# Optimization experiments

Hardware: AMD Instinct MI355X
Metric: run time of the kernel (lower is better)

Reference implementation:

```python
import jax, jax.numpy as jnp
import numpy as np

N_ATOMS = 100_000   # atom_node.size(0)
N_EDGES = 3_200_000  # avg degree 32


def setup_inputs() -> dict:
    key = jax.random.key(0)
    k1, k2, k3, k4, k5 = jax.random.split(key, 5)
    disp = jax.random.normal(k1, (N_EDGES, 3), dtype=jnp.float32)
    a = jax.random.normal(k2, (N_EDGES,), dtype=jnp.float32)
    b = jax.random.normal(k3, (N_EDGES,), dtype=jnp.float32)
    edge_index = jax.random.randint(k4, (2, N_EDGES), 0, N_ATOMS, dtype=jnp.int64)
    atom_node = jax.random.randint(k5, (N_ATOMS,), 0, 100, dtype=jnp.int64)
    return {"disp": disp, "a": a, "b": b, "edge_index": edge_index, "atom_node": atom_node}


def _energy(disp, a, b):
    # surrogate differentiable per-edge energy: E = sum_e a_e*r2_e + b_e*exp(-r2_e)
    r2 = jnp.sum(disp * disp, axis=-1)  # [E]
    return jnp.sum(a * r2 + b * jnp.exp(-r2))


def reference(disp, a, b, edge_index, atom_node):
    n = atom_node.shape[0]
    # force = -dE/d(disp), create_graph analog: jax grads are differentiable
    force_edge = -jax.grad(_energy, argnums=0)(disp, a, b)  # [E,3]
    # dual scatter-add over the two endpoint index rows, then subtract
    f_src = jax.ops.segment_sum(force_edge, edge_index[0], num_segments=n)  # [N,3]
    f_dst = jax.ops.segment_sum(force_edge, edge_index[1], num_segments=n)  # [N,3]
    return f_src - f_dst
```

## Files before the change

kernel.cpp:

```cpp
#include <hip/hip_runtime.h>
#include <hip/hip_bf16.h>
#include <hip/hip_fp16.h>
#include <math.h>
#include <stdint.h>

constexpr int TPB         = 256;
constexpr int U           = 8;
constexpr int EPB         = TPB * U;
constexpr int RECS        = EPB * 2;
constexpr int NPB_SHIFT   = 10;
constexpr int NODES_PER_B = 1 << NPB_SHIFT;
constexpr int NB_MAX      = 128;
constexpr int CAP         = 56;
constexpr int SPLIT       = 8;
constexpr int OCAP        = 262144;

__device__ __forceinline__ uint64_t pack_rec(int local, float fx, float fy, float fz) {
    uint64_t hx = __half_as_ushort(__float2half(fx));
    uint64_t hy = __half_as_ushort(__float2half(fy));
    uint64_t hz = __half_as_ushort(__float2half(fz));
    return (uint64_t)(unsigned)local | (hx << 16) | (hy << 32) | (hz << 48);
}

__global__ void __launch_bounds__(TPB)
p1_partition(const float* __restrict__ disp,
             const float* __restrict__ a,
             const float* __restrict__ b,
             const int* __restrict__ src,
             const int* __restrict__ dst,
             uint64_t* __restrict__ grecords,
             uint4* __restrict__ ovf,
             int* __restrict__ ovf_cnt,
             int E, int NB, int NBLK) {
    __shared__ int      s_cnt[NB_MAX];
    __shared__ int      s_off[NB_MAX];
    __shared__ int      s_gd[NB_MAX];
    __shared__ uint64_t s_rec[RECS];
    __shared__ uint8_t  s_bin[RECS];

    const int t = threadIdx.x;
    const int blk = blockIdx.x;
    const int base = blk * EPB;
    const int bend = min(base + EPB, E);

    if (t < NB_MAX) s_cnt[t] = 0;
    __syncthreads();

    const int e0 = base + t * U;
    float dxv[U], dyv[U], dzv[U], av[U], bv[U];
    int sv[U], dv[U];
    bool valid[U];
    if (e0 + U <= bend) {
        const float4* p = (const float4*)(disp + (size_t)3 * e0);
        float4 q0 = p[0], q1 = p[1], q2 = p[2];
        float4 q3 = p[3], q4 = p[4], q5 = p[5];
        dxv[0] = q0.x; dyv[0] = q0.y; dzv[0] = q0.z;
        dxv[1] = q0.w; dyv[1] = q1.x; dzv[1] = q1.y;
        dxv[2] = q1.z; dyv[2] = q1.w; dzv[2] = q2.x;
        dxv[3] = q2.y; dyv[3] = q2.z; dzv[3] = q2.w;
        dxv[4] = q3.x; dyv[4] = q3.y; dzv[4] = q3.z;
        dxv[5] = q3.w; dyv[5] = q4.x; dzv[5] = q4.y;
        dxv[6] = q4.z; dyv[6] = q4.w; dzv[6] = q5.x;
        dxv[7] = q5.y; dyv[7] = q5.z; dzv[7] = q5.w;
        float4 qa0 = *(const float4*)(a + e0);
        float4 qa1 = *(const float4*)(a + e0 + 4);
        av[0] = qa0.x; av[1] = qa0.y; av[2] = qa0.z; av[3] = qa0.w;
        av[4] = qa1.x; av[5] = qa1.y; av[6] = qa1.z; av[7] = qa1.w;
        float4 qb0 = *(const float4*)(b + e0);
        float4 qb1 = *(const float4*)(b + e0 + 4);
        bv[0] = qb0.x; bv[1] = qb0.y; bv[2] = qb0.z; bv[3] = qb0.w;
        bv[4] = qb1.x; bv[5] = qb1.y; bv[6] = qb1.z; bv[7] = qb1.w;
        int4 qs0 = *(const int4*)(src + e0);
        int4 qs1 = *(const int4*)(src + e0 + 4);
        sv[0] = qs0.x; sv[1] = qs0.y; sv[2] = qs0.z; sv[3] = qs0.w;
        sv[4] = qs1.x; sv[5] = qs1.y; sv[6] = qs1.z; sv[7] = qs1.w;
        int4 qd0 = *(const int4*)(dst + e0);
        int4 qd1 = *(const int4*)(dst + e0 + 4);
        dv[0] = qd0.x; dv[1] = qd0.y; dv[2] = qd0.z; dv[3] = qd0.w;
        dv[4] = qd1.x; dv[5] = qd1.y; dv[6] = qd1.z; dv[7] = qd1.w;
#pragma unroll
        for (int u = 0; u < U; ++u) valid[u] = true;
    } else {
#pragma unroll
        for (int u = 0; u < U; ++u) {
            int e = e0 + u;
            valid[u] = (e < bend);
            if (valid[u]) {
                dxv[u] = disp[3 * e + 0];
                dyv[u] = disp[3 * e + 1];
                dzv[u] = disp[3 * e + 2];
                av[u] = a[e]; bv[u] = b[e];
                sv[u] = src[e]; dv[u] = dst[e];
            }
        }
    }

    uint64_t rec[2 * U];
    int meta[2 * U];
#pragma unroll
    for (int u = 0; u < U; ++u) {
        if (valid[u]) {
            float dx = dxv[u], dy = dyv[u], dz = dzv[u];
            float r2 = dx * dx + dy * dy + dz * dz;
            float coef = -2.0f * (av[u] - bv[u] * __expf(-r2));
            float fx = coef * dx, fy = coef * dy, fz = coef * dz;
            int nds[2] = { sv[u], dv[u] };
#pragma unroll
            for (int j = 0; j < 2; ++j) {
                int k = 2 * u + j;
                float s = j ? -1.0f : 1.0f;
                int node = nds[j];
                rec[k] = pack_rec(node & (NODES_PER_B - 1), s * fx, s * fy, s * fz);
                int bin = node >> NPB_SHIFT;
                int rank = atomicAdd(&s_cnt[bin], 1);
                meta[k] = (bin << 16) | rank;
            }
        } else {
            meta[2 * u] = -1; meta[2 * u + 1] = -1;
        }
    }
    __syncthreads();

    if (t < 64) {
        int v0 = s_cnt[t];
        int v1 = s_cnt[64 + t];
#pragma unroll
        for (int d = 1; d < 64; d <<= 1) {
            int u0 = __shfl_up(v0, d, 64);
            int u1 = __shfl_up(v1, d, 64);
            if (t >= d) { v0 += u0; v1 += u1; }
        }
        int total0 = __shfl(v0, 63, 64);
        s_off[t] = v0;
        s_off[64 + t] = v1 + total0;
    }
    __syncthreads();

    if (t < NB) {
        s_gd[t] = s_cnt[t] - s_off[t];
    }
#pragma unroll
    for (int k = 0; k < 2 * U; ++k) {
        if (meta[k] >= 0) {
            int bin = meta[k] >> 16;
            int rank = meta[k] & 0xFFFF;
            int pos = s_off[bin] - s_cnt[bin] + rank;
            s_rec[pos] = rec[k];
            s_bin[pos] = (uint8_t)bin;
        }
    }
    __syncthreads();

    if (t < NB) {
        uint64_t* seg = grecords + ((size_t)t * NBLK + blk) * CAP;
        for (int p = s_cnt[t]; p < CAP; ++p) seg[p] = 0ull;
    }

    const int total = s_off[NB_MAX - 1];
    for (int i = t; i < total; i += TPB) {
        uint64_t q = s_rec[i];
        int bin = (int)s_bin[i];
        int pos = s_gd[bin] + i;
        if ((unsigned)pos < (unsigned)CAP) {
            grecords[((size_t)bin * NBLK + blk) * CAP + pos] = q;
        } else {
            int o = atomicAdd(ovf_cnt, 1);
            if (o < OCAP) {
                uint4 v;
                v.x = (unsigned)((bin << NPB_SHIFT) | (int)(q & (NODES_PER_B - 1)));
                v.y = __float_as_uint(__half2float(__ushort_as_half((unsigned short)(q >> 16))));
                v.z = __float_as_uint(__half2float(__ushort_as_half((unsigned short)(q >> 32))));
                v.w = __float_as_uint(__half2float(__ushort_as_half((unsigned short)(q >> 48))));
                ovf[o] = v;
            }
        }
    }
}

__device__ __forceinline__ uint64_t enc_xyz(float vx, float vy, float vz) {
    vx = fminf(fmaxf(vx, -63.0f), 63.0f);
    vy = fminf(fmaxf(vy, -63.0f), 63.0f);
    vz = fminf(fmaxf(vz, -63.0f), 63.0f);
    unsigned ex = (unsigned)((int)rintf(vx * 64.0f) + 4096);
    unsigned ey = (unsigned)((int)rintf(vy * 64.0f) + 4096);
    unsigned ez = (unsigned)((int)rintf(vz * 64.0f) + 4096);
    return (1ull << 54) | ((uint64_t)ez << 36) | ((uint64_t)ey << 18) | (uint64_t)ex;
}

__global__ void __launch_bounds__(TPB)
p2_reduce(const uint64_t* __restrict__ grecords,
          float* __restrict__ partials,
          int NB, int NBLK) {
    __shared__ unsigned long long accA[NODES_PER_B];
    const int t = threadIdx.x;
    const int bucket = blockIdx.x >> 3;
    const int part   = blockIdx.x & (SPLIT - 1);

    for (int i = t; i < NODES_PER_B; i += TPB) accA[i] = 0ull;
    __syncthreads();

    const int totslots = NBLK * CAP;
    int lo = (int)((long long)totslots * part / SPLIT);
    int hi = (int)((long long)totslots * (part + 1) / SPLIT);
    const uint64_t* rbase = grecords + (size_t)bucket * totslots;

    int i = lo + t;
    for (; i + 7 * TPB < hi; i += 8 * TPB) {
        uint64_t q[8];
#pragma unroll
        for (int u = 0; u < 8; ++u) q[u] = rbase[i + u * TPB];
#pragma unroll
        for (int u = 0; u < 8; ++u) {
            uint64_t q0 = q[u];
            if (q0 != 0ull) {
                int local = (int)(q0 & (NODES_PER_B - 1));
                float vx = __half2float(__ushort_as_half((unsigned short)(q0 >> 16)));
                float vy = __half2float(__ushort_as_half((unsigned short)(q0 >> 32)));
                float vz = __half2float(__ushort_as_half((unsigned short)(q0 >> 48)));
                atomicAdd(&accA[local], (unsigned long long)enc_xyz(vx, vy, vz));
            }
        }
    }
    for (; i < hi; i += TPB) {
        uint64_t q0 = rbase[i];
        if (q0 != 0ull) {
            int local = (int)(q0 & (NODES_PER_B - 1));
            float vx = __half2float(__ushort_as_half((unsigned short)(q0 >> 16)));
            float vy = __half2float(__ushort_as_half((unsigned short)(q0 >> 32)));
            float vz = __half2float(__ushort_as_half((unsigned short)(q0 >> 48)));
            atomicAdd(&accA[local], (unsigned long long)enc_xyz(vx, vy, vz));
        }
    }
    __syncthreads();

    float* pb = partials + (size_t)part * ((size_t)NB * NODES_PER_B * 3)
              + (size_t)bucket * NODES_PER_B * 3;
    for (int k = t; k < NODES_PER_B; k += TPB) {
        uint64_t A = accA[k];
        float cnt = (float)(unsigned)(A >> 54);
        float xf = (float)(int)(A & 0x3FFFFull);
        float yf = (float)(int)((A >> 18) & 0x3FFFFull);
        float zf = (float)(int)((A >> 36) & 0x3FFFFull);
        float bias = cnt * 4096.0f;
        pb[k * 3 + 0] = (xf - bias) * (1.0f / 64.0f);
        pb[k * 3 + 1] = (yf - bias) * (1.0f / 64.0f);
        pb[k * 3 + 2] = (zf - bias) * (1.0f / 64.0f);
    }
}

__global__ void __launch_bounds__(TPB)
p4_sum_partials(const float* __restrict__ partials, float* __restrict__ out,
                int out_size, size_t pstride) {
    int i = blockIdx.x * blockDim.x + threadIdx.x;
    if (i >= out_size) return;
    float s = 0.0f;
#pragma unroll
    for (int p = 0; p < SPLIT; ++p)
        s += partials[(size_t)p * pstride + i];
    out[i] = s;
}

__global__ void __launch_bounds__(TPB)
p3_overflow(const uint4* __restrict__ ovf, const int* __restrict__ ovf_cnt,
            float* __restrict__ out) {
    int n = *ovf_cnt;
    if (n > OCAP) n = OCAP;
    int stride = gridDim.x * blockDim.x;
    for (int i = blockIdx.x * blockDim.x + threadIdx.x; i < n; i += stride) {
        uint4 r = ovf[i];
        int node = (int)r.x;
        unsafeAtomicAdd(&out[node * 3 + 0], __uint_as_float(r.y));
        unsafeAtomicAdd(&out[node * 3 + 1], __uint_as_float(r.z));
        unsafeAtomicAdd(&out[node * 3 + 2], __uint_as_float(r.w));
    }
}

__global__ void __launch_bounds__(TPB)
edge_force_scatter_direct(const float* __restrict__ disp,
                          const float* __restrict__ a,
                          const float* __restrict__ b,
                          const int* __restrict__ src,
                          const int* __restrict__ dst,
                          float* __restrict__ out,
                          int E) {
    int e = blockIdx.x * blockDim.x + threadIdx.x;
    if (e >= E) return;
    float dx = disp[3 * e + 0], dy = disp[3 * e + 1], dz = disp[3 * e + 2];
    float r2 = dx * dx + dy * dy + dz * dz;
    float coef = -2.0f * (a[e] - b[e] * __expf(-r2));
    float fx = coef * dx, fy = coef * dy, fz = coef * dz;
    int s = 3 * src[e], d = 3 * dst[e];
    unsafeAtomicAdd(&out[s + 0], fx);
    unsafeAtomicAdd(&out[s + 1], fy);
    unsafeAtomicAdd(&out[s + 2], fz);
    unsafeAtomicAdd(&out[d + 0], -fx);
    unsafeAtomicAdd(&out[d + 1], -fy);
    unsafeAtomicAdd(&out[d + 2], -fz);
}

extern "C" void kernel_launch(void* const* d_in, const int* in_sizes, int n_in,
                              void* d_out, int out_size, void* d_ws, size_t ws_size,
                              hipStream_t stream) {
    const float* disp = (const float*)d_in[0];
    const float* a    = (const float*)d_in[1];
    const float* b    = (const float*)d_in[2];
    const int*   ei   = (const int*)d_in[3];

    int E = in_sizes[1];
    int N = in_sizes[4];
    float* out = (float*)d_out;

    int NB = (N + NODES_PER_B - 1) >> NPB_SHIFT;
    int NBLK = (E + EPB - 1) / EPB;
    size_t pstride = (size_t)NB * NODES_PER_B * 3;

    size_t rec_bytes  = (size_t)NB * NBLK * CAP * sizeof(uint64_t);
    size_t need = 256
                + rec_bytes
                + (size_t)OCAP * sizeof(uint4)
                + (size_t)SPLIT * pstride * sizeof(float);

    if (NB <= NB_MAX && ws_size >= need) {
        char* wsb = (char*)d_ws;
        int* ovf_cnt       = (int*)wsb;
        uint64_t* grecords = (uint64_t*)(wsb + 256);
        uint4* ovf         = (uint4*)(wsb + 256 + rec_bytes);
        float* partials    = (float*)((char*)ovf + (size_t)OCAP * sizeof(uint4));

        (void)hipMemsetAsync(wsb, 0, 256, stream);

        p1_partition<<<NBLK, TPB, 0, stream>>>(
            disp, a, b, ei, ei + E, grecords, ovf, ovf_cnt, E, NB, NBLK);
        p2_reduce<<<NB * SPLIT, TPB, 0, stream>>>(
            grecords, partials, NB, NBLK);
        int grid4 = (out_size + TPB - 1) / TPB;
        p4_sum_partials<<<grid4, TPB, 0, stream>>>(partials, out, out_size, pstride);
        p3_overflow<<<64, TPB, 0, stream>>>(ovf, ovf_cnt, out);
    } else {
        (void)hipMemsetAsync(d_out, 0, (size_t)out_size * sizeof(float), stream);
        int grid = (E + TPB - 1) / TPB;
        edge_force_scatter_direct<<<grid, TPB, 0, stream>>>(
            disp, a, b, ei, ei + E, out, E);
    }
}
```

Measured before the change: 166.2 us.

## Fuse partial summation and overflow handling into reduce kernel via last-block ticket

```diff
diff --git a/kernel.cpp b/kernel.cpp
--- a/kernel.cpp
+++ b/kernel.cpp
@@ -188,13 +188,19 @@
 }
 
 __global__ void __launch_bounds__(TPB)
-p2_reduce(const uint64_t* __restrict__ grecords,
-          float* __restrict__ partials,
-          int NB, int NBLK) {
+p2_reduce_fused(const uint64_t* __restrict__ grecords,
+                const uint4* __restrict__ ovf,
+                const int* __restrict__ ovf_cnt,
+                int* __restrict__ done,
+                float* __restrict__ partials,
+                float* __restrict__ out,
+                int N, int NB, int NBLK) {
     __shared__ unsigned long long accA[NODES_PER_B];
+    __shared__ int s_tick;
     const int t = threadIdx.x;
     const int bucket = blockIdx.x >> 3;
     const int part   = blockIdx.x & (SPLIT - 1);
+    const size_t pstride = (size_t)NB * NODES_PER_B * 3;
 
     for (int i = t; i < NODES_PER_B; i += TPB) accA[i] = 0ull;
     __syncthreads();
@@ -233,7 +239,7 @@
     }
     __syncthreads();
 
-    float* pb = partials + (size_t)part * ((size_t)NB * NODES_PER_B * 3)
+    float* pb = partials + (size_t)part * pstride
               + (size_t)bucket * NODES_PER_B * 3;
     for (int k = t; k < NODES_PER_B; k += TPB) {
         uint64_t A = accA[k];
@@ -246,32 +252,50 @@
         pb[k * 3 + 1] = (yf - bias) * (1.0f / 64.0f);
         pb[k * 3 + 2] = (zf - bias) * (1.0f / 64.0f);
     }
-}
-
-__global__ void __launch_bounds__(TPB)
-p4_sum_partials(const float* __restrict__ partials, float* __restrict__ out,
-                int out_size, size_t pstride) {
-    int i = blockIdx.x * blockDim.x + threadIdx.x;
-    if (i >= out_size) return;
-    float s = 0.0f;
-#pragma unroll
-    for (int p = 0; p < SPLIT; ++p)
-        s += partials[(size_t)p * pstride + i];
-    out[i] = s;
-}
-
-__global__ void __launch_bounds__(TPB)
-p3_overflow(const uint4* __restrict__ ovf, const int* __restrict__ ovf_cnt,
-            float* __restrict__ out) {
+
+    __threadfence();
+    __syncthreads();
+    if (t == 0) s_tick = atomicAdd(&done[bucket], 1);
+    __syncthreads();
+    if (s_tick != SPLIT - 1) return;
+
+    __threadfence();
+
+    for (int k = t; k < NODES_PER_B; k += TPB) accA[k] = 0ull;
+    __syncthreads();
     int n = *ovf_cnt;
     if (n > OCAP) n = OCAP;
-    int stride = gridDim.x * blockDim.x;
-    for (int i = blockIdx.x * blockDim.x + threadIdx.x; i < n; i += stride) {
-        uint4 r = ovf[i];
+    for (int k = t; k < n; k += TPB) {
+        uint4 r = ovf[k];
         int node = (int)r.x;
-        unsafeAtomicAdd(&out[node * 3 + 0], __uint_as_float(r.y));
-        unsafeAtomicAdd(&out[node * 3 + 1], __uint_as_float(r.z));
-        unsafeAtomicAdd(&out[node * 3 + 2], __uint_as_float(r.w));
+        if ((node >> NPB_SHIFT) == bucket) {
+            atomicAdd(&accA[node & (NODES_PER_B - 1)],
+                      (unsigned long long)enc_xyz(__uint_as_float(r.y),
+                                                  __uint_as_float(r.z),
+                                                  __uint_as_float(r.w)));
+        }
+    }
+    __syncthreads();
+
+    const int nbase = bucket << NPB_SHIFT;
+    const int nmax  = min(NODES_PER_B, N - nbase);
+    const float* pbb = partials + (size_t)bucket * NODES_PER_B * 3;
+    for (int k = t; k < nmax; k += TPB) {
+        float sx = 0.0f, sy = 0.0f, sz = 0.0f;
+#pragma unroll
+        for (int p = 0; p < SPLIT; ++p) {
+            const float* q = pbb + (size_t)p * pstride + (size_t)k * 3;
+            sx += q[0]; sy += q[1]; sz += q[2];
+        }
+        uint64_t A = accA[k];
+        float cnt = (float)(unsigned)(A >> 54);
+        float bias = cnt * 4096.0f;
+        sx += ((float)(int)(A & 0x3FFFFull)         - bias) * (1.0f / 64.0f);
+        sy += ((float)(int)((A >> 18) & 0x3FFFFull) - bias) * (1.0f / 64.0f);
+        sz += ((float)(int)((A >> 36) & 0x3FFFFull) - bias) * (1.0f / 64.0f);
+        out[(size_t)(nbase + k) * 3 + 0] = sx;
+        out[(size_t)(nbase + k) * 3 + 1] = sy;
+        out[(size_t)(nbase + k) * 3 + 2] = sz;
     }
 }
 
@@ -315,27 +339,25 @@
     size_t pstride = (size_t)NB * NODES_PER_B * 3;
 
     size_t rec_bytes  = (size_t)NB * NBLK * CAP * sizeof(uint64_t);
-    size_t need = 256
+    size_t need = 1024
                 + rec_bytes
                 + (size_t)OCAP * sizeof(uint4)
                 + (size_t)SPLIT * pstride * sizeof(float);
 
-    if (NB <= NB_MAX && ws_size >= need) {
+    if (NB <= NB_MAX && NB <= 512 && ws_size >= need) {
         char* wsb = (char*)d_ws;
         int* ovf_cnt       = (int*)wsb;
-        uint64_t* grecords = (uint64_t*)(wsb + 256);
-        uint4* ovf         = (uint4*)(wsb + 256 + rec_bytes);
+        int* done          = (int*)(wsb + 128);
+        uint64_t* grecords = (uint64_t*)(wsb + 1024);
+        uint4* ovf         = (uint4*)(wsb + 1024 + rec_bytes);
         float* partials    = (float*)((char*)ovf + (size_t)OCAP * sizeof(uint4));
 
-        (void)hipMemsetAsync(wsb, 0, 256, stream);
+        (void)hipMemsetAsync(wsb, 0, 1024, stream);
 
         p1_partition<<<NBLK, TPB, 0, stream>>>(
             disp, a, b, ei, ei + E, grecords, ovf, ovf_cnt, E, NB, NBLK);
-        p2_reduce<<<NB * SPLIT, TPB, 0, stream>>>(
-            grecords, partials, NB, NBLK);
-        int grid4 = (out_size + TPB - 1) / TPB;
-        p4_sum_partials<<<grid4, TPB, 0, stream>>>(partials, out, out_size, pstride);
-        p3_overflow<<<64, TPB, 0, stream>>>(ovf, ovf_cnt, out);
+        p2_reduce_fused<<<NB * SPLIT, TPB, 0, stream>>>(
+            grecords, ovf, ovf_cnt, done, partials, out, N, NB, NBLK);
     } else {
         (void)hipMemsetAsync(d_out, 0, (size_t)out_size * sizeof(float), stream);
         int grid = (E + TPB - 1) / TPB;
```

After: 256.0 us. 1.54x slower.

## Scatter records directly to global bins, dropping shared-memory staging and prefix scan

Applied to the files above, without the earlier changes.

```diff
diff --git a/kernel.cpp b/kernel.cpp
--- a/kernel.cpp
+++ b/kernel.cpp
@@ -6,12 +6,12 @@
 
 constexpr int TPB         = 256;
 constexpr int U           = 8;
-constexpr int EPB         = TPB * U;
-constexpr int RECS        = EPB * 2;
+constexpr int ROUNDS      = 2;
+constexpr int EPB         = TPB * U * ROUNDS;
 constexpr int NPB_SHIFT   = 10;
 constexpr int NODES_PER_B = 1 << NPB_SHIFT;
 constexpr int NB_MAX      = 128;
-constexpr int CAP         = 56;
+constexpr int CAP         = 96;
 constexpr int SPLIT       = 8;
 constexpr int OCAP        = 262144;
 
@@ -32,11 +32,7 @@
              uint4* __restrict__ ovf,
              int* __restrict__ ovf_cnt,
              int E, int NB, int NBLK) {
-    __shared__ int      s_cnt[NB_MAX];
-    __shared__ int      s_off[NB_MAX];
-    __shared__ int      s_gd[NB_MAX];
-    __shared__ uint64_t s_rec[RECS];
-    __shared__ uint8_t  s_bin[RECS];
+    __shared__ int s_cnt[NB_MAX];
 
     const int t = threadIdx.x;
     const int blk = blockIdx.x;
@@ -46,60 +42,61 @@
     if (t < NB_MAX) s_cnt[t] = 0;
     __syncthreads();
 
-    const int e0 = base + t * U;
-    float dxv[U], dyv[U], dzv[U], av[U], bv[U];
-    int sv[U], dv[U];
-    bool valid[U];
-    if (e0 + U <= bend) {
-        const float4* p = (const float4*)(disp + (size_t)3 * e0);
-        float4 q0 = p[0], q1 = p[1], q2 = p[2];
-        float4 q3 = p[3], q4 = p[4], q5 = p[5];
-        dxv[0] = q0.x; dyv[0] = q0.y; dzv[0] = q0.z;
-        dxv[1] = q0.w; dyv[1] = q1.x; dzv[1] = q1.y;
-        dxv[2] = q1.z; dyv[2] = q1.w; dzv[2] = q2.x;
-        dxv[3] = q2.y; dyv[3] = q2.z; dzv[3] = q2.w;
-        dxv[4] = q3.x; dyv[4] = q3.y; dzv[4] = q3.z;
-        dxv[5] = q3.w; dyv[5] = q4.x; dzv[5] = q4.y;
-        dxv[6] = q4.z; dyv[6] = q4.w; dzv[6] = q5.x;
-        dxv[7] = q5.y; dyv[7] = q5.z; dzv[7] = q5.w;
-        float4 qa0 = *(const float4*)(a + e0);
-        float4 qa1 = *(const float4*)(a + e0 + 4);
-        av[0] = qa0.x; av[1] = qa0.y; av[2] = qa0.z; av[3] = qa0.w;
-        av[4] = qa1.x; av[5] = qa1.y; av[6] = qa1.z; av[7] = qa1.w;
-        float4 qb0 = *(const float4*)(b + e0);
-        float4 qb1 = *(const float4*)(b + e0 + 4);
-        bv[0] = qb0.x; bv[1] = qb0.y; bv[2] = qb0.z; bv[3] = qb0.w;
-        bv[4] = qb1.x; bv[5] = qb1.y; bv[6] = qb1.z; bv[7] = qb1.w;
-        int4 qs0 = *(const int4*)(src + e0);
-        int4 qs1 = *(const int4*)(src + e0 + 4);
-        sv[0] = qs0.x; sv[1] = qs0.y; sv[2] = qs0.z; sv[3] = qs0.w;
-        sv[4] = qs1.x; sv[5] = qs1.y; sv[6] = qs1.z; sv[7] = qs1.w;
-        int4 qd0 = *(const int4*)(dst + e0);
-        int4 qd1 = *(const int4*)(dst + e0 + 4);
-        dv[0] = qd0.x; dv[1] = qd0.y; dv[2] = qd0.z; dv[3] = qd0.w;
-        dv[4] = qd1.x; dv[5] = qd1.y; dv[6] = qd1.z; dv[7] = qd1.w;
-#pragma unroll
-        for (int u = 0; u < U; ++u) valid[u] = true;
-    } else {
-#pragma unroll
-        for (int u = 0; u < U; ++u) {
-            int e = e0 + u;
-            valid[u] = (e < bend);
-            if (valid[u]) {
-                dxv[u] = disp[3 * e + 0];
-                dyv[u] = disp[3 * e + 1];
-                dzv[u] = disp[3 * e + 2];
-                av[u] = a[e]; bv[u] = b[e];
-                sv[u] = src[e]; dv[u] = dst[e];
+    for (int r = 0; r < ROUNDS; ++r) {
+        const int e0 = base + r * TPB * U + t * U;
+        if (e0 >= bend) break;
+
+        float dxv[U], dyv[U], dzv[U], av[U], bv[U];
+        int sv[U], dv[U];
+        bool valid[U];
+        if (e0 + U <= bend) {
+            const float4* p = (const float4*)(disp + (size_t)3 * e0);
+            float4 q0 = p[0], q1 = p[1], q2 = p[2];
+            float4 q3 = p[3], q4 = p[4], q5 = p[5];
+            dxv[0] = q0.x; dyv[0] = q0.y; dzv[0] = q0.z;
+            dxv[1] = q0.w; dyv[1] = q1.x; dzv[1] = q1.y;
+            dxv[2] = q1.z; dyv[2] = q1.w; dzv[2] = q2.x;
+            dxv[3] = q2.y; dyv[3] = q2.z; dzv[3] = q2.w;
+            dxv[4] = q3.x; dyv[4] = q3.y; dzv[4] = q3.z;
+            dxv[5] = q3.w; dyv[5] = q4.x; dzv[5] = q4.y;
+            dxv[6] = q4.z; dyv[6] = q4.w; dzv[6] = q5.x;
+            dxv[7] = q5.y; dyv[7] = q5.z; dzv[7] = q5.w;
+            float4 qa0 = *(const float4*)(a + e0);
+            float4 qa1 = *(const float4*)(a + e0 + 4);
+            av[0] = qa0.x; av[1] = qa0.y; av[2] = qa0.z; av[3] = qa0.w;
+            av[4] = qa1.x; av[5] = qa1.y; av[6] = qa1.z; av[7] = qa1.w;
+            float4 qb0 = *(const float4*)(b + e0);
+            float4 qb1 = *(const float4*)(b + e0 + 4);
+            bv[0] = qb0.x; bv[1] = qb0.y; bv[2] = qb0.z; bv[3] = qb0.w;
+            bv[4] = qb1.x; bv[5] = qb1.y; bv[6] = qb1.z; bv[7] = qb1.w;
+            int4 qs0 = *(const int4*)(src + e0);
+            int4 qs1 = *(const int4*)(src + e0 + 4);
+            sv[0] = qs0.x; sv[1] = qs0.y; sv[2] = qs0.z; sv[3] = qs0.w;
+            sv[4] = qs1.x; sv[5] = qs1.y; sv[6] = qs1.z; sv[7] = qs1.w;
+            int4 qd0 = *(const int4*)(dst + e0);
+            int4 qd1 = *(const int4*)(dst + e0 + 4);
+            dv[0] = qd0.x; dv[1] = qd0.y; dv[2] = qd0.z; dv[3] = qd0.w;
+            dv[4] = qd1.x; dv[5] = qd1.y; dv[6] = qd1.z; dv[7] = qd1.w;
+#pragma unroll
+            for (int u = 0; u < U; ++u) valid[u] = true;
+        } else {
+#pragma unroll
+            for (int u = 0; u < U; ++u) {
+                int e = e0 + u;
+                valid[u] = (e < bend);
+                if (valid[u]) {
+                    dxv[u] = disp[3 * e + 0];
+                    dyv[u] = disp[3 * e + 1];
+                    dzv[u] = disp[3 * e + 2];
+                    av[u] = a[e]; bv[u] = b[e];
+                    sv[u] = src[e]; dv[u] = dst[e];
+                }
             }
         }
-    }
-
-    uint64_t rec[2 * U];
-    int meta[2 * U];
-#pragma unroll
-    for (int u = 0; u < U; ++u) {
-        if (valid[u]) {
+
+#pragma unroll
+        for (int u = 0; u < U; ++u) {
+            if (!valid[u]) continue;
             float dx = dxv[u], dy = dyv[u], dz = dzv[u];
             float r2 = dx * dx + dy * dy + dz * dz;
             float coef = -2.0f * (av[u] - bv[u] * __expf(-r2));
@@ -107,73 +104,33 @@
             int nds[2] = { sv[u], dv[u] };
 #pragma unroll
             for (int j = 0; j < 2; ++j) {
-                int k = 2 * u + j;
                 float s = j ? -1.0f : 1.0f;
                 int node = nds[j];
-                rec[k] = pack_rec(node & (NODES_PER_B - 1), s * fx, s * fy, s * fz);
                 int bin = node >> NPB_SHIFT;
                 int rank = atomicAdd(&s_cnt[bin], 1);
-                meta[k] = (bin << 16) | rank;
-            }
-        } else {
-            meta[2 * u] = -1; meta[2 * u + 1] = -1;
-        }
-    }
-    __syncthreads();
-
-    if (t < 64) {
-        int v0 = s_cnt[t];
-        int v1 = s_cnt[64 + t];
-#pragma unroll
-        for (int d = 1; d < 64; d <<= 1) {
-            int u0 = __shfl_up(v0, d, 64);
-            int u1 = __shfl_up(v1, d, 64);
-            if (t >= d) { v0 += u0; v1 += u1; }
-        }
-        int total0 = __shfl(v0, 63, 64);
-        s_off[t] = v0;
-        s_off[64 + t] = v1 + total0;
-    }
-    __syncthreads();
-
-    if (t < NB) {
-        s_gd[t] = s_cnt[t] - s_off[t];
-    }
-#pragma unroll
-    for (int k = 0; k < 2 * U; ++k) {
-        if (meta[k] >= 0) {
-            int bin = meta[k] >> 16;
-            int rank = meta[k] & 0xFFFF;
-            int pos = s_off[bin] - s_cnt[bin] + rank;
-            s_rec[pos] = rec[k];
-            s_bin[pos] = (uint8_t)bin;
-        }
-    }
-    __syncthreads();
-
-    if (t < NB) {
-        uint64_t* seg = grecords + ((size_t)t * NBLK + blk) * CAP;
-        for (int p = s_cnt[t]; p < CAP; ++p) seg[p] = 0ull;
-    }
-
-    const int total = s_off[NB_MAX - 1];
-    for (int i = t; i < total; i += TPB) {
-        uint64_t q = s_rec[i];
-        int bin = (int)s_bin[i];
-        int pos = s_gd[bin] + i;
-        if ((unsigned)pos < (unsigned)CAP) {
-            grecords[((size_t)bin * NBLK + blk) * CAP + pos] = q;
-        } else {
-            int o = atomicAdd(ovf_cnt, 1);
-            if (o < OCAP) {
-                uint4 v;
-                v.x = (unsigned)((bin << NPB_SHIFT) | (int)(q & (NODES_PER_B - 1)));
-                v.y = __float_as_uint(__half2float(__ushort_as_half((unsigned short)(q >> 16))));
-                v.z = __float_as_uint(__half2float(__ushort_as_half((unsigned short)(q >> 32))));
-                v.w = __float_as_uint(__half2float(__ushort_as_half((unsigned short)(q >> 48))));
-                ovf[o] = v;
+                if (rank < CAP) {
+                    grecords[((size_t)bin * NBLK + blk) * CAP + rank] =
+                        pack_rec(node & (NODES_PER_B - 1), s * fx, s * fy, s * fz);
+                } else {
+                    int o = atomicAdd(ovf_cnt, 1);
+                    if (o < OCAP) {
+                        uint4 v;
+                        v.x = (unsigned)node;
+                        v.y = __float_as_uint(s * fx);
+                        v.z = __float_as_uint(s * fy);
+                        v.w = __float_as_uint(s * fz);
+                        ovf[o] = v;
+                    }
+                }
             }
         }
+    }
+    __syncthreads();
+
+    if (t < NB) {
+        int c = min(s_cnt[t], CAP);
+        uint64_t* seg = grecords + ((size_t)t * NBLK + blk) * CAP;
+        for (int p = c; p < CAP; ++p) seg[p] = 0ull;
     }
 }
 
```

Result: slower. 279.3 us (+68.0%).
